# Optimization experiments

Hardware: AMD Instinct MI355X
Metric: run time of the kernel (lower is better)

Reference implementation:

```python
import jax, jax.numpy as jnp
import numpy as np

B, T, V, E, H, C = 64, 512, 100000, 300, 128, 20  # H = hidden//2 per direction


def setup_inputs() -> dict:
    key = jax.random.key(0)
    ks = jax.random.split(key, 16)
    s = 0.05
    x = jax.random.randint(ks[0], (B, T), 0, V)
    lengths = jax.random.randint(ks[1], (B,), T // 4, T + 1)
    mask = jnp.arange(T)[None, :] < lengths[:, None]           # [B,T] bool
    tags = jax.random.randint(ks[2], (B, T), 0, C)
    emb = (jax.random.normal(ks[3], (V, E)) * s).at[0].set(0.0)  # padding_idx=0 zeroed
    W_ih_f = jax.random.normal(ks[4], (4 * H, E)) * s
    W_hh_f = jax.random.normal(ks[5], (4 * H, H)) * s
    b_ih_f = jax.random.normal(ks[6], (4 * H,)) * s
    b_hh_f = jax.random.normal(ks[7], (4 * H,)) * s
    W_ih_b = jax.random.normal(ks[8], (4 * H, E)) * s
    W_hh_b = jax.random.normal(ks[9], (4 * H, H)) * s
    b_ih_b = jax.random.normal(ks[10], (4 * H,)) * s
    b_hh_b = jax.random.normal(ks[11], (4 * H,)) * s
    fc_W = jax.random.normal(ks[12], (C, 2 * H)) * s
    fc_b = jax.random.normal(ks[13], (C,)) * s
    transitions = jax.random.uniform(ks[14], (C, C), minval=-0.1, maxval=0.1)
    return dict(x=x, mask=mask, tags=tags, emb=emb,
                W_ih_f=W_ih_f, W_hh_f=W_hh_f, b_ih_f=b_ih_f, b_hh_f=b_hh_f,
                W_ih_b=W_ih_b, W_hh_b=W_hh_b, b_ih_b=b_ih_b, b_hh_b=b_hh_b,
                fc_W=fc_W, fc_b=fc_b, transitions=transitions)


def _lstm_dir(xe, W_ih, W_hh, b_ih, b_hh):
    # xe: [B,T,E]; torch LSTM gate order i,f,g,o
    b, t, _ = xe.shape
    h_dim = W_hh.shape[1]
    xw = jnp.einsum('bte,ge->btg', xe, W_ih) + b_ih + b_hh      # [B,T,4H]

    def step(carry, xw_t):
        h, c = carry
        g = xw_t + h @ W_hh.T
        i, f, gg, o = jnp.split(g, 4, axis=-1)
        i = jax.nn.sigmoid(i); f = jax.nn.sigmoid(f)
        gg = jnp.tanh(gg); o = jax.nn.sigmoid(o)
        c = f * c + i * gg
        h = o * jnp.tanh(c)
        return (h, c), h

    init = (jnp.zeros((b, h_dim), xe.dtype), jnp.zeros((b, h_dim), xe.dtype))
    _, hs = jax.lax.scan(step, init, jnp.swapaxes(xw, 0, 1))    # [T,B,H]
    return jnp.swapaxes(hs, 0, 1)


def _crf_nll(logits, tags, mask, transitions):
    maskf = mask.astype(logits.dtype)
    # log partition (forward algorithm)
    em_t = jnp.swapaxes(logits, 0, 1)                           # [T,B,C]
    m_t = jnp.swapaxes(mask, 0, 1)                              # [T,B]

    def part_step(log_alpha, inp):
        emit_t, mt = inp
        scores = log_alpha[:, :, None] + transitions[None] + emit_t[:, None, :]
        la = jax.nn.logsumexp(scores, axis=1)
        return jnp.where(mt[:, None], la, log_alpha), None

    log_alpha, _ = jax.lax.scan(part_step, em_t[0], (em_t[1:], m_t[1:]))
    log_den = jax.nn.logsumexp(log_alpha, axis=1)               # [B]
    # joint log likelihood of gold path
    emit_score = jnp.take_along_axis(logits, tags[..., None], axis=2)[..., 0]
    pair = transitions[tags[:, :-1], tags[:, 1:]]               # [B,T-1]
    pm = (mask[:, 1:] & mask[:, :-1]).astype(logits.dtype)
    log_num = (emit_score * maskf).sum(axis=1) + (pair * pm).sum(axis=1)
    return jnp.mean(log_den - log_num)


def reference(x, mask, tags, emb, W_ih_f, W_hh_f, b_ih_f, b_hh_f,
              W_ih_b, W_hh_b, b_ih_b, b_hh_b, fc_W, fc_b, transitions):
    xe = emb[x]                                                 # [B,T,E]
    h_f = _lstm_dir(xe, W_ih_f, W_hh_f, b_ih_f, b_hh_f)
    h_b = _lstm_dir(xe[:, ::-1], W_ih_b, W_hh_b, b_ih_b, b_hh_b)[:, ::-1]
    out = jnp.concatenate([h_f, h_b], axis=-1)                  # [B,T,2H]
    logits = out @ fc_W.T + fc_b                                # [B,T,C]
    loss = _crf_nll(logits, tags, mask, transitions)
    return loss, logits
```

## Files before the change

kernel.cpp:

```cpp
#include <hip/hip_runtime.h>
#include <hip/hip_bf16.h>

typedef unsigned short u16;
typedef unsigned char u8;
typedef unsigned int u32;
typedef __attribute__((ext_vector_type(8))) short short8;
typedef __attribute__((ext_vector_type(4))) float f32x4;

#define B_ 64
#define T_ 512
#define E_ 300
#define KP_ 320
#define H_ 128
#define G_ 512
#define C_ 20
#define NCH_ 32
#define CS_ 16

__device__ __forceinline__ float b2f(u16 u) {
    union { u32 i; float f; } v; v.i = ((u32)u) << 16; return v.f;
}
__device__ __forceinline__ u16 f2b(float f) {
    union { float f; u32 i; } v; v.f = f;
    u32 r = (v.i + 0x7fffu + ((v.i >> 16) & 1u)) >> 16;
    return (u16)r;
}
__device__ __forceinline__ float loadf(const void* p, long i, u32 isf32) {
    return isf32 ? ((const float*)p)[i] : b2f(((const u16*)p)[i]);
}
__device__ __forceinline__ float sigmoidf_(float x) {
    return 1.0f / (1.0f + __expf(-x));
}
__device__ __forceinline__ float tanhf_(float x) {
    float cx = fminf(fmaxf(x, -15.f), 15.f);
    float e = __expf(2.f * cx);
    return (e - 1.f) / (e + 1.f);
}
__device__ __forceinline__ int loadmask(const void* m, int idx, u32 isbool) {
    return isbool ? (int)((const u8*)m)[idx] : ((const int*)m)[idx];
}

__global__ void sniff_kernel(const u32* __restrict__ emb32,
                             const u32* __restrict__ mask32,
                             u32* __restrict__ flags) {
    if (threadIdx.x == 0) {
        u32 nz = 0;
        for (int i = 150; i < 300; ++i) nz |= emb32[i];
        flags[0] = (nz == 0) ? 1u : 0u;
        u32 m0 = mask32[0];
        flags[1] = ((m0 & 0xFFFFFF00u) != 0) ? 1u : 0u;
    }
}

__global__ __launch_bounds__(256) void prep_kernel(
    const void* __restrict__ Wihf, const void* __restrict__ Wihb,
    const void* __restrict__ Whhf, const void* __restrict__ Whhb,
    const void* __restrict__ bihf, const void* __restrict__ bhhf,
    const void* __restrict__ bihb, const void* __restrict__ bhhb,
    const void* __restrict__ fcW, const void* __restrict__ fcb,
    const void* __restrict__ trans, const u32* __restrict__ flags,
    u16* __restrict__ Wpad, u16* __restrict__ Whhc, float* __restrict__ biasc,
    u16* __restrict__ fcWc, float* __restrict__ fcbf, float* __restrict__ transf) {
    const u32 isf32 = flags[0];
    int idx = blockIdx.x * 256 + threadIdx.x;
    if (idx < 2 * G_ * KP_) {
        int dir = idx / (G_ * KP_), rem = idx % (G_ * KP_);
        int g = rem / KP_, kp = rem % KP_;
        const void* src = dir ? Wihb : Wihf;
        float v = (kp < E_) ? loadf(src, (long)g * E_ + kp, isf32) : 0.f;
        Wpad[idx] = f2b(v);
        return;
    }
    idx -= 2 * G_ * KP_;
    if (idx < 2 * G_ * H_) {
        int dir = idx >> 16, r = idx & 65535;
        Whhc[idx] = f2b(loadf(dir ? Whhb : Whhf, r, isf32));
        return;
    }
    idx -= 2 * G_ * H_;
    if (idx < 2 * G_) {
        int dir = idx >> 9, g = idx & 511;
        biasc[idx] = loadf(dir ? bihb : bihf, g, isf32) +
                     loadf(dir ? bhhb : bhhf, g, isf32);
        return;
    }
    idx -= 2 * G_;
    if (idx < C_ * 256) { fcWc[idx] = f2b(loadf(fcW, idx, isf32)); return; }
    idx -= C_ * 256;
    if (idx < C_) { fcbf[idx] = loadf(fcb, idx, isf32); return; }
    idx -= C_;
    if (idx < C_ * C_) { transf[idx] = loadf(trans, idx, isf32); return; }
}

__global__ __launch_bounds__(256) void gemm_xw(const int* __restrict__ x,
                                               const void* __restrict__ emb,
                                               const u16* __restrict__ Wpad,
                                               const float* __restrict__ biasc,
                                               const u32* __restrict__ flags,
                                               u16* __restrict__ xwf, u16* __restrict__ xwb,
                                               int tclog2, int t0f, int t0b) {
    const int m0 = blockIdx.x * 128;
    const int n0 = blockIdx.y * 128;
    const int dir = blockIdx.z;
    const u16* Bw = Wpad + (size_t)dir * G_ * KP_;
    u16* out = dir ? xwb : xwf;
    const int t0 = dir ? t0b : t0f;
    const int ts = dir ? -1 : 1;
    const int tcm = (1 << tclog2) - 1;
    const u32 isf32 = flags[0];

    __shared__ __align__(16) short As[128 * 32];
    __shared__ __align__(16) short Bs[128 * 32];
    __shared__ int xs[128];

    const int tid = threadIdx.x;
    const int lane = tid & 63;
    const int wave = tid >> 6;
    const int wm = wave & 1, wn = wave >> 1;
    const int lr = lane & 15, lq = lane >> 4;

    if (tid < 128) {
        int i = m0 + tid;
        int b = i >> tclog2;
        int r = i & tcm;
        xs[tid] = x[b * T_ + t0 + ts * r];
    }
    __syncthreads();

    f32x4 acc[4][4];
#pragma unroll
    for (int mt = 0; mt < 4; ++mt)
#pragma unroll
        for (int nt = 0; nt < 4; ++nt)
            acc[mt][nt] = (f32x4){0.f, 0.f, 0.f, 0.f};

    for (int kb = 0; kb < KP_; kb += 32) {
        if (isf32) {
            const float* ef = (const float*)emb;
#pragma unroll
            for (int hh = 0; hh < 4; ++hh) {
                int c = tid + hh * 256;
                int row = c >> 3;
                int k4 = (c & 7) * 4;
                int k = kb + k4;
                uint2 o = make_uint2(0u, 0u);
                if (k < E_) {
                    float4 v = *(const float4*)(ef + (size_t)xs[row] * E_ + k);
                    o.x = (u32)f2b(v.x) | ((u32)f2b(v.y) << 16);
                    o.y = (u32)f2b(v.z) | ((u32)f2b(v.w) << 16);
                }
                *(uint2*)(&As[row * 32 + k4]) = o;
            }
        } else {
            const u16* eb = (const u16*)emb;
#pragma unroll
            for (int hh = 0; hh < 4; ++hh) {
                int c = tid + hh * 256;
                int row = c >> 3;
                int k4 = (c & 7) * 4;
                int k = kb + k4;
                uint2 va = make_uint2(0u, 0u);
                if (k < E_)
                    va = *(const uint2*)(eb + (size_t)xs[row] * E_ + k);
                *(uint2*)(&As[row * 32 + k4]) = va;
            }
        }
#pragma unroll
        for (int hh = 0; hh < 2; ++hh) {
            int c = tid + hh * 256;
            int row = c >> 2;
            int k8 = (c & 3) * 8;
            uint4 vb = *(const uint4*)(Bw + (size_t)(n0 + row) * KP_ + kb + k8);
            *(uint4*)(&Bs[row * 32 + k8]) = vb;
        }
        __syncthreads();
        short8 afr[4], bfr[4];
#pragma unroll
        for (int mt = 0; mt < 4; ++mt)
            afr[mt] = *(const short8*)&As[(wm * 64 + mt * 16 + lr) * 32 + lq * 8];
#pragma unroll
        for (int nt = 0; nt < 4; ++nt)
            bfr[nt] = *(const short8*)&Bs[(wn * 64 + nt * 16 + lr) * 32 + lq * 8];
#pragma unroll
        for (int mt = 0; mt < 4; ++mt)
#pragma unroll
            for (int nt = 0; nt < 4; ++nt)
                acc[mt][nt] = __builtin_amdgcn_mfma_f32_16x16x32_bf16(afr[mt], bfr[nt], acc[mt][nt], 0, 0, 0);
        __syncthreads();
    }
#pragma unroll
    for (int nt = 0; nt < 4; ++nt) {
        int n = n0 + wn * 64 + nt * 16 + lr;
        float bn = biasc[dir * G_ + n];
#pragma unroll
        for (int mt = 0; mt < 4; ++mt) {
            int mbase = m0 + wm * 64 + mt * 16 + lq * 4;
#pragma unroll
            for (int r = 0; r < 4; ++r)
                out[(size_t)(mbase + r) * G_ + n] = f2b(acc[mt][nt][r] + bn);
        }
    }
}

__global__ __launch_bounds__(512) void lstm_kernel(const u16* __restrict__ Whhc,
                                                   const u16* __restrict__ xwf,
                                                   const u16* __restrict__ xwb,
                                                   u16* __restrict__ hf,
                                                   u16* __restrict__ hb,
                                                   float* __restrict__ carry,
                                                   int TC, int t0f, int t0b, int first) {
    const int b = blockIdx.x;
    const int dir = blockIdx.y;
    const int j = threadIdx.x;
    const u16* W = Whhc + (size_t)dir * G_ * H_ + (size_t)j * H_;
    const u16* xw = (dir ? xwb : xwf) + (size_t)b * TC * G_;
    u16* hout = (dir ? hb : hf) + (size_t)b * T_ * H_;
    const int t0 = dir ? t0b : t0f;
    const int ts = dir ? -1 : 1;
    float* carry_c = carry + (size_t)(dir * B_ + b) * H_;
    float* carry_h = carry + (size_t)(2 * B_ + dir * B_ + b) * H_;

    float Wr[H_];
#pragma unroll
    for (int k = 0; k < H_; k += 8) {
        uint4 v = *(const uint4*)(W + k);
        Wr[k + 0] = b2f((u16)(v.x & 0xffff)); Wr[k + 1] = b2f((u16)(v.x >> 16));
        Wr[k + 2] = b2f((u16)(v.y & 0xffff)); Wr[k + 3] = b2f((u16)(v.y >> 16));
        Wr[k + 4] = b2f((u16)(v.z & 0xffff)); Wr[k + 5] = b2f((u16)(v.z >> 16));
        Wr[k + 6] = b2f((u16)(v.w & 0xffff)); Wr[k + 7] = b2f((u16)(v.w >> 16));
    }

    __shared__ float hs[H_];
    __shared__ float gs[G_];
    float c = 0.f;
    if (j < H_) {
        if (first) { hs[j] = 0.f; c = 0.f; }
        else       { hs[j] = carry_h[j]; c = carry_c[j]; }
    }
    __syncthreads();

    const bool is_g = (j >= 256) && (j < 384);
    for (int r = 0; r < TC; ++r) {
        float xv = b2f(xw[(size_t)r * G_ + j]);
        float acc = 0.f;
#pragma unroll
        for (int kc = 0; kc < H_; kc += 16) {
#pragma unroll
            for (int k = 0; k < 16; ++k)
                acc += Wr[kc + k] * hs[kc + k];
        }
        float g = xv + acc;
        gs[j] = is_g ? tanhf_(g) : sigmoidf_(g);
        __syncthreads();
        if (j < H_) {
            float ig = gs[j], fg = gs[H_ + j], gg = gs[2 * H_ + j], og = gs[3 * H_ + j];
            c = fg * c + ig * gg;
            float h = og * tanhf_(c);
            hs[j] = h;
            int tg = t0 + ts * r;
            hout[(size_t)tg * H_ + j] = f2b(h);
        }
        __syncthreads();
    }
    if (j < H_) { carry_c[j] = c; carry_h[j] = hs[j]; }
}

__global__ __launch_bounds__(256) void fc_kernel(const u16* __restrict__ hf,
                                                 const u16* __restrict__ hb,
                                                 const u16* __restrict__ fcWc,
                                                 const float* __restrict__ fcbf,
                                                 const u32* __restrict__ flags,
                                                 float* __restrict__ logits,
                                                 void* __restrict__ dout) {
    __shared__ float Ws[C_ * 256];
    __shared__ float Hs[16 * 256];
    const int tid = threadIdx.x;
    const int bt0 = blockIdx.x * 64;
    const u32 isf32 = flags[0];
#pragma unroll
    for (int i = 0; i < C_; ++i) {
        int v = tid + i * 256;
        Ws[v] = b2f(fcWc[v]);
    }
    __syncthreads();
    for (int grp = 0; grp < 4; ++grp) {
        int btg = bt0 + grp * 16;
#pragma unroll
        for (int i = 0; i < 16; ++i) {
            int v = tid + i * 256;
            int r = v >> 8, k = v & 255;
            Hs[v] = (k < H_) ? b2f(hf[(size_t)(btg + r) * H_ + k])
                             : b2f(hb[(size_t)(btg + r) * H_ + (k - H_)]);
        }
        __syncthreads();
#pragma unroll
        for (int q = 0; q < 2; ++q) {
            int p = tid + q * 256;
            if (p < 16 * C_) {
                int r = p / C_, cc = p % C_;
                float acc = fcbf[cc];
                const float* wr = &Ws[cc * 256];
                const float* hr = &Hs[r * 256];
#pragma unroll
                for (int k = 0; k < 256; k += 4)
                    acc += wr[k] * hr[k] + wr[k + 1] * hr[k + 1] +
                           wr[k + 2] * hr[k + 2] + wr[k + 3] * hr[k + 3];
                size_t o = (size_t)(btg + r) * C_ + cc;
                logits[o] = acc;
                if (isf32) ((float*)dout)[1 + o] = acc;
                else       ((u16*)dout)[1 + o] = f2b(acc);
            }
        }
        __syncthreads();
    }
}

__global__ __launch_bounds__(512) void crf_chunk(const float* __restrict__ logits,
                                                 const void* __restrict__ mask,
                                                 const float* __restrict__ transf,
                                                 const u32* __restrict__ flags,
                                                 float* __restrict__ Mc) {
    const int c = blockIdx.x;
    const int b = blockIdx.y;
    const int p = threadIdx.x;
    const bool act = p < C_ * C_;
    const int i = p / C_, j = p % C_;
    const u32 isbool = flags[1];

    __shared__ float P[C_ * C_];
    float trj[C_];
    if (act) {
#pragma unroll
        for (int k = 0; k < C_; ++k) trj[k] = transf[k * C_ + j];
        P[p] = (i == j) ? 0.f : -1e30f;
    }
    __syncthreads();

    const float* lg = logits + (size_t)b * T_ * C_;
    const int t0 = 1 + CS_ * c;

    float e = 0.f; int mk = 0;
    if (act) e = lg[(size_t)t0 * C_ + j];
    mk = loadmask(mask, b * T_ + t0, isbool);

    for (int s = 0; s < CS_; ++s) {
        int t = t0 + s;
        if (t >= T_) break;
        float e_n = 0.f; int mk_n = 0;
        int tn = t + 1;
        if (s + 1 < CS_ && tn < T_) {
            if (act) e_n = lg[(size_t)tn * C_ + j];
            mk_n = loadmask(mask, b * T_ + tn, isbool);
        }
        float nv = 0.f;
        if (act) {
            float sv[C_];
            float mx = -3e38f;
#pragma unroll
            for (int k = 0; k < C_; ++k) {
                sv[k] = P[i * C_ + k] + trj[k];
                mx = fmaxf(mx, sv[k]);
            }
            float sum = 0.f;
#pragma unroll
            for (int k = 0; k < C_; ++k) sum += __expf(sv[k] - mx);
            float la = mx + __logf(sum) + e;
            nv = mk ? la : P[p];
        }
        __syncthreads();
        if (act) P[p] = nv;
        __syncthreads();
        e = e_n; mk = mk_n;
    }
    if (act) Mc[((size_t)b * NCH_ + c) * (C_ * C_) + p] = P[p];
}

__global__ __launch_bounds__(64) void crf_combine(const float* __restrict__ logits,
                                                  const float* __restrict__ Mc,
                                                  float* __restrict__ log_den) {
    const int b = blockIdx.x;
    const int j = threadIdx.x;
    const bool act = j < C_;
    __shared__ float alpha[C_];
    const float* lg = logits + (size_t)b * T_ * C_;
    const float* mb = Mc + (size_t)b * NCH_ * (C_ * C_);
    if (act) alpha[j] = lg[j];
    __syncthreads();

    float mc[C_], mcn[C_];
    if (act) {
#pragma unroll
        for (int i = 0; i < C_; ++i) mc[i] = mb[i * C_ + j];
    }
    for (int c = 0; c < NCH_; ++c) {
        if (act && c + 1 < NCH_) {
#pragma unroll
            for (int i = 0; i < C_; ++i) mcn[i] = mb[(size_t)(c + 1) * (C_ * C_) + i * C_ + j];
        }
        float nv = 0.f;
        if (act) {
            float sv[C_];
            float mx = -3e38f;
#pragma unroll
            for (int i = 0; i < C_; ++i) {
                sv[i] = alpha[i] + mc[i];
                mx = fmaxf(mx, sv[i]);
            }
            float sum = 0.f;
#pragma unroll
            for (int i = 0; i < C_; ++i) sum += __expf(sv[i] - mx);
            nv = mx + __logf(sum);
        }
        __syncthreads();
        if (act) alpha[j] = nv;
        __syncthreads();
#pragma unroll
        for (int i = 0; i < C_; ++i) mc[i] = mcn[i];
    }
    if (j == 0) {
        float mx = -3e38f;
#pragma unroll
        for (int i = 0; i < C_; ++i) mx = fmaxf(mx, alpha[i]);
        float sum = 0.f;
#pragma unroll
        for (int i = 0; i < C_; ++i) sum += __expf(alpha[i] - mx);
        log_den[b] = mx + __logf(sum);
    }
}

__global__ __launch_bounds__(64) void loss_partial(const float* __restrict__ logits,
                                                   const void* __restrict__ mask,
                                                   const int* __restrict__ tags,
                                                   const float* __restrict__ transf,
                                                   const u32* __restrict__ flags,
                                                   float* __restrict__ num) {
    const int b = blockIdx.x;
    const int lane = threadIdx.x;
    const u32 isbool = flags[1];
    const float* lg = logits + (size_t)b * T_ * C_;
    const int* tg = tags + b * T_;
    float s = 0.f;
    for (int t = lane; t < T_; t += 64) {
        int tt = tg[t];
        int mm = loadmask(mask, b * T_ + t, isbool);
        if (mm) s += lg[(size_t)t * C_ + tt];
        if (t >= 1) {
            int tp = tg[t - 1];
            int mp = loadmask(mask, b * T_ + t - 1, isbool);
            if (mm && mp) s += transf[tp * C_ + tt];
        }
    }
#pragma unroll
    for (int off = 32; off >= 1; off >>= 1)
        s += __shfl_down(s, off, 64);
    if (lane == 0) num[b] = s;
}

__global__ __launch_bounds__(64) void loss_final(const float* __restrict__ den,
                                                 const float* __restrict__ num,
                                                 const u32* __restrict__ flags,
                                                 void* __restrict__ dout) {
    const int b = threadIdx.x;
    float v = den[b] - num[b];
#pragma unroll
    for (int off = 32; off >= 1; off >>= 1)
        v += __shfl_down(v, off, 64);
    if (b == 0) {
        float loss = v * (1.0f / B_);
        if (flags[0]) ((float*)dout)[0] = loss;
        else          ((u16*)dout)[0] = f2b(loss);
    }
}

extern "C" void kernel_launch(void* const* d_in, const int* in_sizes, int n_in,
                              void* d_out, int out_size, void* d_ws, size_t ws_size,
                              hipStream_t stream) {
    const int* x     = (const int*)d_in[0];
    const void* mask = d_in[1];
    const int* tags  = (const int*)d_in[2];
    const void* emb  = d_in[3];
    const void* Wihf = d_in[4];
    const void* Whhf = d_in[5];
    const void* bihf = d_in[6];
    const void* bhhf = d_in[7];
    const void* Wihb = d_in[8];
    const void* Whhb = d_in[9];
    const void* bihb = d_in[10];
    const void* bhhb = d_in[11];
    const void* fcW  = d_in[12];
    const void* fcb  = d_in[13];
    const void* trans= d_in[14];

    char* ws = (char*)d_ws;
    u32*   flags = (u32*)(ws + 0);
    u16*   Wpad  = (u16*)(ws + 256);
    u16*   Whhc  = (u16*)(ws + 655616);
    float* biasc = (float*)(ws + 917760);
    u16*   fcWc  = (u16*)(ws + 921856);
    float* fcbf  = (float*)(ws + 932096);
    float* transf= (float*)(ws + 932224);
    u16*   hf    = (u16*)(ws + 933888);
    u16*   hb    = (u16*)(ws + 9322496);
    float* lgf   = (float*)(ws + 17711104);
    float* den   = (float*)(ws + 20332544);
    float* carry = (float*)(ws + 20332800);
    float* Mc    = (float*)(ws + 20463872);
    float* numb  = (float*)(ws + 23740672);
    const size_t xw_off = 23740928;

    int TC, lg2;
    if (ws_size >= xw_off + 2ull * 65536ull * 128ull + 4096ull)      { TC = 128; lg2 = 7; }
    else if (ws_size >= xw_off + 2ull * 65536ull * 64ull + 4096ull)  { TC = 64;  lg2 = 6; }
    else                                                             { TC = 32;  lg2 = 5; }
    u16* xwf = (u16*)(ws + xw_off);
    u16* xwb = (u16*)(ws + xw_off + (size_t)65536 * TC);

    hipLaunchKernelGGL(sniff_kernel, dim3(1), dim3(64), 0, stream,
                       (const u32*)emb, (const u32*)mask, flags);
    hipLaunchKernelGGL(prep_kernel, dim3(1818), dim3(256), 0, stream,
                       Wihf, Wihb, Whhf, Whhb, bihf, bhhf, bihb, bhhb,
                       fcW, fcb, trans, flags, Wpad, Whhc, biasc, fcWc, fcbf, transf);

    const int nc = T_ / TC;
    for (int ci = 0; ci < nc; ++ci) {
        int t0f = ci * TC;
        int t0b = T_ - 1 - ci * TC;
        hipLaunchKernelGGL(gemm_xw, dim3((B_ * TC) / 128, 4, 2), dim3(256), 0, stream,
                           x, emb, Wpad, biasc, flags, xwf, xwb, lg2, t0f, t0b);
        hipLaunchKernelGGL(lstm_kernel, dim3(B_, 2), dim3(512), 0, stream,
                           Whhc, xwf, xwb, hf, hb, carry, TC, t0f, t0b, (ci == 0) ? 1 : 0);
    }

    hipLaunchKernelGGL(fc_kernel, dim3(512), dim3(256), 0, stream,
                       hf, hb, fcWc, fcbf, flags, lgf, d_out);
    hipLaunchKernelGGL(crf_chunk, dim3(NCH_, B_), dim3(512), 0, stream,
                       lgf, mask, transf, flags, Mc);
    hipLaunchKernelGGL(crf_combine, dim3(B_), dim3(64), 0, stream, lgf, Mc, den);
    hipLaunchKernelGGL(loss_partial, dim3(B_), dim3(64), 0, stream,
                       lgf, mask, tags, transf, flags, numb);
    hipLaunchKernelGGL(loss_final, dim3(1), dim3(64), 0, stream, den, numb, flags, d_out);
}
```

Before: 904.3 us.

## Interleave LSTM gate rows per hidden unit and exchange gates via wave shuffles

The recurrent LSTM kernel now maps each group of four adjacent threads to the i/f/g/o gate rows of one hidden unit, so the gates are combined with wave shuffles instead of a shared-memory gate buffer. This removes one of the two block barriers per timestep. The hidden state is double-buffered in LDS and read as float4, the next step's input projection is prefetched, and the dot product is split into four accumulators. Every thread now redundantly computes the cell update, and occupancy hints are added through launch bounds.

Result: slower. 1.018 ms (+12.6%).

```diff
diff --git a/kernel.cpp b/kernel.cpp
--- a/kernel.cpp
+++ b/kernel.cpp
@@ -202,18 +202,21 @@
     }
 }
 
-__global__ __launch_bounds__(512) void lstm_kernel(const u16* __restrict__ Whhc,
-                                                   const u16* __restrict__ xwf,
-                                                   const u16* __restrict__ xwb,
-                                                   u16* __restrict__ hf,
-                                                   u16* __restrict__ hb,
-                                                   float* __restrict__ carry,
-                                                   int TC, int t0f, int t0b, int first) {
+__global__ __launch_bounds__(512, 2) void lstm_kernel(const u16* __restrict__ Whhc,
+                                                      const u16* __restrict__ xwf,
+                                                      const u16* __restrict__ xwb,
+                                                      u16* __restrict__ hf,
+                                                      u16* __restrict__ hb,
+                                                      float* __restrict__ carry,
+                                                      int TC, int t0f, int t0b, int first) {
     const int b = blockIdx.x;
     const int dir = blockIdx.y;
-    const int j = threadIdx.x;
-    const u16* W = Whhc + (size_t)dir * G_ * H_ + (size_t)j * H_;
-    const u16* xw = (dir ? xwb : xwf) + (size_t)b * TC * G_;
+    const int tid = threadIdx.x;
+    const int j = tid >> 2;
+    const int gq = tid & 3;
+    const int row = gq * H_ + j;
+    const u16* W = Whhc + (size_t)dir * G_ * H_ + (size_t)row * H_;
+    const u16* xw = (dir ? xwb : xwf) + (size_t)b * TC * G_ + row;
     u16* hout = (dir ? hb : hf) + (size_t)b * T_ * H_;
     const int t0 = dir ? t0b : t0f;
     const int ts = dir ? -1 : 1;
@@ -230,39 +233,46 @@
         Wr[k + 6] = b2f((u16)(v.w & 0xffff)); Wr[k + 7] = b2f((u16)(v.w >> 16));
     }
 
-    __shared__ float hs[H_];
-    __shared__ float gs[G_];
-    float c = 0.f;
-    if (j < H_) {
-        if (first) { hs[j] = 0.f; c = 0.f; }
-        else       { hs[j] = carry_h[j]; c = carry_c[j]; }
-    }
+    __shared__ float hs[2][H_];
+    float c = first ? 0.f : carry_c[j];
+    if (tid < H_) hs[0][tid] = first ? 0.f : carry_h[tid];
     __syncthreads();
 
-    const bool is_g = (j >= 256) && (j < 384);
+    const int lane = tid & 63;
+    const int lbase = lane & ~3;
+    int cur = 0;
+    float xv = b2f(xw[0]);
     for (int r = 0; r < TC; ++r) {
-        float xv = b2f(xw[(size_t)r * G_ + j]);
-        float acc = 0.f;
-#pragma unroll
-        for (int kc = 0; kc < H_; kc += 16) {
-#pragma unroll
-            for (int k = 0; k < 16; ++k)
-                acc += Wr[kc + k] * hs[kc + k];
-        }
-        float g = xv + acc;
-        gs[j] = is_g ? tanhf_(g) : sigmoidf_(g);
-        __syncthreads();
-        if (j < H_) {
-            float ig = gs[j], fg = gs[H_ + j], gg = gs[2 * H_ + j], og = gs[3 * H_ + j];
-            c = fg * c + ig * gg;
-            float h = og * tanhf_(c);
-            hs[j] = h;
+        float xv_n = 0.f;
+        if (r + 1 < TC) xv_n = b2f(xw[(size_t)(r + 1) * G_]);
+        const float* hsp = hs[cur];
+        float a0 = 0.f, a1 = 0.f, a2 = 0.f, a3 = 0.f;
+#pragma unroll
+        for (int k = 0; k < H_; k += 4) {
+            float4 hv = *(const float4*)&hsp[k];
+            a0 += Wr[k + 0] * hv.x;
+            a1 += Wr[k + 1] * hv.y;
+            a2 += Wr[k + 2] * hv.z;
+            a3 += Wr[k + 3] * hv.w;
+        }
+        float g = xv + ((a0 + a1) + (a2 + a3));
+        float v = (gq == 2) ? tanhf_(g) : sigmoidf_(g);
+        float vi = __shfl(v, lbase + 0, 64);
+        float vf = __shfl(v, lbase + 1, 64);
+        float vg = __shfl(v, lbase + 2, 64);
+        float vo = __shfl(v, lbase + 3, 64);
+        c = vf * c + vi * vg;
+        float h = vo * tanhf_(c);
+        if (gq == 0) {
+            hs[cur ^ 1][j] = h;
             int tg = t0 + ts * r;
             hout[(size_t)tg * H_ + j] = f2b(h);
         }
         __syncthreads();
-    }
-    if (j < H_) { carry_c[j] = c; carry_h[j] = hs[j]; }
+        cur ^= 1;
+        xv = xv_n;
+    }
+    if (gq == 0) { carry_c[j] = c; carry_h[j] = hs[cur][j]; }
 }
 
 __global__ __launch_bounds__(256) void fc_kernel(const u16* __restrict__ hf,
```
